# Kernel tuning notes

Hardware: AMD Instinct MI355X
Metric: run time of the kernel (lower is better)

## Reference

```python
import jax, jax.numpy as jnp
import numpy as np

K = 256  # k winners per row


def setup_inputs() -> dict:
    key = jax.random.key(0)
    k1, k2 = jax.random.split(key)
    x = jax.random.normal(k1, (32768, 2048), dtype=jnp.float32)
    importance = jax.random.normal(k2, (2048,), dtype=jnp.float32)
    return {"x": x, "importance": importance}


def reference(x, importance):
    # scores = |x| * |importance|  (broadcast over batch)
    scores = jnp.abs(x) * jnp.abs(importance)
    # top-k indices per row, then scatter 1.0 into a zero mask
    _, idx = jax.lax.top_k(scores, K)              # [B, K]
    rows = jnp.arange(x.shape[0])[:, None]          # [B, 1]
    mask = jnp.zeros_like(x).at[rows, idx].set(1.0)
    return x * mask
```

## Files before the change

### kernel.cpp

```cpp
#include <hip/hip_runtime.h>

#define COLS 2048
#define KSEL 256
#define TPB  256

#define WOFF  1024
#define BC    1028
#define BC2   1032
#define CNTW  1036
#define BUF   1040
#define R2O   1296
#define NWORDS 1360

__device__ __forceinline__ unsigned mbcnt64(unsigned long long m) {
    unsigned c = __builtin_amdgcn_mbcnt_lo((unsigned)m, 0u);
    return __builtin_amdgcn_mbcnt_hi((unsigned)(m >> 32), c);
}

__global__ __launch_bounds__(TPB)
void CompetitiveSelection_topk_kernel(const float* __restrict__ x,
                                      const float* __restrict__ imp,
                                      float* __restrict__ out)
{
    __shared__ __align__(16) unsigned lds[NWORDS];
    const int tid  = threadIdx.x;
    const int lane = tid & 63;
    const int wid  = tid >> 6;
    const long base = (long)blockIdx.x * COLS + tid * 8;

    *(uint4*)&lds[4 * tid] = make_uint4(0, 0, 0, 0);
    if (tid == 0) lds[CNTW] = 0;
    __syncthreads();

    float4 xa = *(const float4*)(x + base);
    float4 xb = *(const float4*)(x + base + 4);
    float4 ia = *(const float4*)(imp + tid * 8);
    float4 ib = *(const float4*)(imp + tid * 8 + 4);
    float xs[8] = {xa.x, xa.y, xa.z, xa.w, xb.x, xb.y, xb.z, xb.w};
    float iv[8] = {ia.x, ia.y, ia.z, ia.w, ib.x, ib.y, ib.z, ib.w};
    unsigned sc[8];
#pragma unroll
    for (int j = 0; j < 8; ++j) {
        sc[j] = __float_as_uint(xs[j] * iv[j]) & 0x7FFFFFFFu;
        atomicAdd(&lds[sc[j] >> 21], 1u);
    }
    __syncthreads();

    unsigned T = 0, kk = KSEL, na = 0;
    unsigned hm = 0x80000000u;
    int nb = 31;

    auto passScan = [&](int s) {
        uint4 h = *(const uint4*)&lds[4 * tid];
        unsigned cnt[4] = {h.x, h.y, h.z, h.w};
        unsigned tot = cnt[0] + cnt[1] + cnt[2] + cnt[3];
        unsigned S = tot;
#pragma unroll
        for (int off = 1; off < 64; off <<= 1) {
            unsigned u = __shfl_down(S, off);
            if (lane + off < 64) S += u;
        }
        if (lane == 0) lds[WOFF + wid] = S;
        __syncthreads();
        unsigned above = S - tot;
#pragma unroll
        for (int w = 0; w < 4; ++w) above += (w > wid) ? lds[WOFF + w] : 0u;
        int cc = -1; unsigned cab = 0, cnb = 0;
#pragma unroll
        for (int b = 3; b >= 0; --b) {
            if (cc < 0 && above < kk && above + cnt[b] >= kk) {
                cc = 4 * tid + b; cab = above; cnb = cnt[b];
            }
            above += cnt[b];
        }
        if (cc >= 0) {
            lds[BC + 0] = T | ((unsigned)cc << s);
            lds[BC + 1] = kk - cab;
            lds[BC + 2] = cnb;
        }
        __syncthreads();
        T = lds[BC + 0]; kk = lds[BC + 1]; na = lds[BC + 2];
        hm |= (0x3FFu << s);
        nb = s;
    };

    passScan(21);

    while (na > 256u && nb > 0) {
        int s = (nb > 10) ? (nb - 10) : 0;
        *(uint4*)&lds[4 * tid] = make_uint4(0, 0, 0, 0);
        __syncthreads();
#pragma unroll
        for (int j = 0; j < 8; ++j)
            if ((sc[j] & hm) == T) atomicAdd(&lds[(sc[j] >> s) & 1023u], 1u);
        __syncthreads();
        passScan(s);
    }

    unsigned ne, nlist = 0;
    if (nb == 0) {
        ne = na;
    } else {
        {
            unsigned c = 0;
#pragma unroll
            for (int j = 0; j < 8; ++j) c += ((sc[j] & hm) == T) ? 1u : 0u;
            unsigned S = c;
#pragma unroll
            for (int off = 1; off < 64; off <<= 1) {
                unsigned u = __shfl_up(S, off);
                if (lane >= off) S += u;
            }
            unsigned rb = 0;
            if (lane == 63) rb = atomicAdd(&lds[CNTW], S);
            unsigned p = BUF + __shfl(rb, 63) + S - c;
#pragma unroll
            for (int j = 0; j < 8; ++j)
                if ((sc[j] & hm) == T) lds[p++] = sc[j];
            nlist = na;
        }
        __syncthreads();

        while (na > 64u && nb > 0) {
            int s = (nb > 10) ? (nb - 10) : 0;
            *(uint4*)&lds[4 * tid] = make_uint4(0, 0, 0, 0);
            __syncthreads();
            for (int idx = tid; idx < (int)nlist; idx += TPB) {
                unsigned v = lds[BUF + idx];
                if ((v & hm) == T) atomicAdd(&lds[(v >> s) & 1023u], 1u);
            }
            __syncthreads();
            passScan(s);
        }

        if (nb == 0) {
            ne = na;
        } else {
            if (wid == 0) {
                unsigned run2 = 0;
                const unsigned nit = (nlist + 63u) >> 6;
                for (unsigned k = 0; k < nit; ++k) {
                    unsigned idx = (unsigned)lane + 64u * k;
                    bool inb = idx < nlist;
                    unsigned v = inb ? lds[BUF + idx] : 0u;
                    bool act = inb && ((v & hm) == T);
                    unsigned long long m = __ballot(act);
                    if (act) lds[R2O + run2 + mbcnt64(m)] = v;
                    run2 += (unsigned)__popcll(m);
                }
                unsigned v = ((unsigned)lane < na) ? lds[R2O + lane] : 0u;
                unsigned long long M = __ballot((unsigned)lane < na);
                unsigned tl = 0, k2 = kk;
                for (int b = nb - 1; b >= 0; --b) {
                    unsigned long long ones = __ballot((v >> b) & 1u) & M;
                    unsigned c1 = (unsigned)__popcll(ones);
                    if (c1 >= k2) { M = ones; tl |= (1u << b); }
                    else          { M &= ~ones; k2 -= c1; }
                }
                if (lane == 0) {
                    lds[BC2 + 0] = T | tl;
                    lds[BC2 + 1] = k2;
                    lds[BC2 + 2] = (unsigned)__popcll(M);
                }
            }
            __syncthreads();
            T = lds[BC2 + 0]; kk = lds[BC2 + 1]; ne = lds[BC2 + 2];
        }
    }

    float* orow = out + base;
    if (ne == kk) {
        float4 oa, ob;
        oa.x = (sc[0] >= T) ? xs[0] : 0.0f;
        oa.y = (sc[1] >= T) ? xs[1] : 0.0f;
        oa.z = (sc[2] >= T) ? xs[2] : 0.0f;
        oa.w = (sc[3] >= T) ? xs[3] : 0.0f;
        ob.x = (sc[4] >= T) ? xs[4] : 0.0f;
        ob.y = (sc[5] >= T) ? xs[5] : 0.0f;
        ob.z = (sc[6] >= T) ? xs[6] : 0.0f;
        ob.w = (sc[7] >= T) ? xs[7] : 0.0f;
        *(float4*)(orow)     = oa;
        *(float4*)(orow + 4) = ob;
    } else {
        unsigned eq = 0;
#pragma unroll
        for (int j = 0; j < 8; ++j) eq += (sc[j] == T) ? 1u : 0u;
        unsigned S = eq;
#pragma unroll
        for (int off = 1; off < 64; off <<= 1) {
            unsigned u = __shfl_up(S, off);
            if (lane >= off) S += u;
        }
        if (lane == 63) lds[WOFF + wid] = S;
        __syncthreads();
        unsigned add = 0;
#pragma unroll
        for (int w = 0; w < 4; ++w) add += (w < wid) ? lds[WOFF + w] : 0u;
        unsigned ebase = add + S - eq;
        float o[8];
#pragma unroll
        for (int j = 0; j < 8; ++j) {
            bool pick = sc[j] > T;
            if (sc[j] == T) { pick = (ebase < kk); ebase += 1; }
            o[j] = pick ? xs[j] : 0.0f;
        }
        *(float4*)(orow)     = make_float4(o[0], o[1], o[2], o[3]);
        *(float4*)(orow + 4) = make_float4(o[4], o[5], o[6], o[7]);
    }
}

extern "C" void kernel_launch(void* const* d_in, const int* in_sizes, int n_in,
                              void* d_out, int out_size, void* d_ws, size_t ws_size,
                              hipStream_t stream)
{
    const float* x   = (const float*)d_in[0];
    const float* imp = (const float*)d_in[1];
    float* out       = (float*)d_out;

    const int rows = in_sizes[0] / COLS;
    CompetitiveSelection_topk_kernel<<<dim3(rows), dim3(TPB), 0, stream>>>(x, imp, out);
}
```

Before: 111.4 us.

## Process two rows per block with interleaved radix-select passes

Each block now handles two rows, running their histogram and scan passes side by side so the two rows share barriers and have more independent work in flight. The refinement loop now stays on register-held scores until at most 64 candidates remain, dropping the intermediate LDS candidate list and the extra compaction step. The grid is halved. In exchange, registers per thread and LDS per block grow, and a row that needs more passes than its partner leaves that partner idle in the lockstep loop.

```diff
diff --git a/kernel.cpp b/kernel.cpp
--- a/kernel.cpp
+++ b/kernel.cpp
@@ -4,18 +4,19 @@
 #define KSEL 256
 #define TPB  256
 
-#define WOFF  1024
-#define BC    1028
-#define BC2   1032
-#define CNTW  1036
-#define BUF   1040
-#define R2O   1296
-#define NWORDS 1360
-
-__device__ __forceinline__ unsigned mbcnt64(unsigned long long m) {
-    unsigned c = __builtin_amdgcn_mbcnt_lo((unsigned)m, 0u);
-    return __builtin_amdgcn_mbcnt_hi((unsigned)(m >> 32), c);
-}
+#define HA    0
+#define HB    1024
+#define WOFFA 2048
+#define WOFFB 2052
+#define BCA   2056
+#define BCB   2060
+#define BC2A  2064
+#define BC2B  2068
+#define CA    2072
+#define CB    2073
+#define BUFA  2080
+#define BUFB  2144
+#define NWORDS 2208
 
 __global__ __launch_bounds__(TPB)
 void CompetitiveSelection_topk_kernel(const float* __restrict__ x,
@@ -26,186 +27,267 @@
     const int tid  = threadIdx.x;
     const int lane = tid & 63;
     const int wid  = tid >> 6;
-    const long base = (long)blockIdx.x * COLS + tid * 8;
-
-    *(uint4*)&lds[4 * tid] = make_uint4(0, 0, 0, 0);
-    if (tid == 0) lds[CNTW] = 0;
+    const long baseA = (long)(2 * blockIdx.x) * COLS + tid * 8;
+    const long baseB = baseA + COLS;
+
+    const uint4 z4 = make_uint4(0, 0, 0, 0);
+    *(uint4*)&lds[HA + 4 * tid] = z4;
+    *(uint4*)&lds[HB + 4 * tid] = z4;
+    if (tid < 2) lds[CA + tid] = 0;
     __syncthreads();
 
-    float4 xa = *(const float4*)(x + base);
-    float4 xb = *(const float4*)(x + base + 4);
-    float4 ia = *(const float4*)(imp + tid * 8);
-    float4 ib = *(const float4*)(imp + tid * 8 + 4);
-    float xs[8] = {xa.x, xa.y, xa.z, xa.w, xb.x, xb.y, xb.z, xb.w};
-    float iv[8] = {ia.x, ia.y, ia.z, ia.w, ib.x, ib.y, ib.z, ib.w};
-    unsigned sc[8];
+    float4 a0 = *(const float4*)(x + baseA);
+    float4 a1 = *(const float4*)(x + baseA + 4);
+    float4 b0 = *(const float4*)(x + baseB);
+    float4 b1 = *(const float4*)(x + baseB + 4);
+    float4 i0 = *(const float4*)(imp + tid * 8);
+    float4 i1 = *(const float4*)(imp + tid * 8 + 4);
+    float xsA[8] = {a0.x, a0.y, a0.z, a0.w, a1.x, a1.y, a1.z, a1.w};
+    float xsB[8] = {b0.x, b0.y, b0.z, b0.w, b1.x, b1.y, b1.z, b1.w};
+    float ivv[8] = {i0.x, i0.y, i0.z, i0.w, i1.x, i1.y, i1.z, i1.w};
+    unsigned scA[8], scB[8];
 #pragma unroll
     for (int j = 0; j < 8; ++j) {
-        sc[j] = __float_as_uint(xs[j] * iv[j]) & 0x7FFFFFFFu;
-        atomicAdd(&lds[sc[j] >> 21], 1u);
+        scA[j] = __float_as_uint(xsA[j] * ivv[j]) & 0x7FFFFFFFu;
+        scB[j] = __float_as_uint(xsB[j] * ivv[j]) & 0x7FFFFFFFu;
+        atomicAdd(&lds[HA + (scA[j] >> 21)], 1u);
+        atomicAdd(&lds[HB + (scB[j] >> 21)], 1u);
     }
     __syncthreads();
 
-    unsigned T = 0, kk = KSEL, na = 0;
-    unsigned hm = 0x80000000u;
-    int nb = 31;
-
-    auto passScan = [&](int s) {
-        uint4 h = *(const uint4*)&lds[4 * tid];
-        unsigned cnt[4] = {h.x, h.y, h.z, h.w};
-        unsigned tot = cnt[0] + cnt[1] + cnt[2] + cnt[3];
-        unsigned S = tot;
-#pragma unroll
-        for (int off = 1; off < 64; off <<= 1) {
-            unsigned u = __shfl_down(S, off);
-            if (lane + off < 64) S += u;
-        }
-        if (lane == 0) lds[WOFF + wid] = S;
-        __syncthreads();
-        unsigned above = S - tot;
-#pragma unroll
-        for (int w = 0; w < 4; ++w) above += (w > wid) ? lds[WOFF + w] : 0u;
-        int cc = -1; unsigned cab = 0, cnb = 0;
-#pragma unroll
-        for (int b = 3; b >= 0; --b) {
-            if (cc < 0 && above < kk && above + cnt[b] >= kk) {
-                cc = 4 * tid + b; cab = above; cnb = cnt[b];
-            }
-            above += cnt[b];
-        }
-        if (cc >= 0) {
-            lds[BC + 0] = T | ((unsigned)cc << s);
-            lds[BC + 1] = kk - cab;
-            lds[BC + 2] = cnb;
-        }
-        __syncthreads();
-        T = lds[BC + 0]; kk = lds[BC + 1]; na = lds[BC + 2];
-        hm |= (0x3FFu << s);
-        nb = s;
+    unsigned TA = 0, kkA = KSEL, naA = 0, hmA = 0x80000000u;
+    unsigned TB = 0, kkB = KSEL, naB = 0, hmB = 0x80000000u;
+    int nbA = 31, nbB = 31;
+
+    auto scanBoth = [&](bool actA, int sA, bool actB, int sB) {
+        uint4 hA4, hB4; unsigned SA = 0, SB = 0, totA = 0, totB = 0;
+        if (actA) {
+            hA4 = *(const uint4*)&lds[HA + 4 * tid];
+            totA = hA4.x + hA4.y + hA4.z + hA4.w; SA = totA;
+#pragma unroll
+            for (int off = 1; off < 64; off <<= 1) {
+                unsigned u = __shfl_down(SA, off);
+                if (lane + off < 64) SA += u;
+            }
+            if (lane == 0) lds[WOFFA + wid] = SA;
+        }
+        if (actB) {
+            hB4 = *(const uint4*)&lds[HB + 4 * tid];
+            totB = hB4.x + hB4.y + hB4.z + hB4.w; SB = totB;
+#pragma unroll
+            for (int off = 1; off < 64; off <<= 1) {
+                unsigned u = __shfl_down(SB, off);
+                if (lane + off < 64) SB += u;
+            }
+            if (lane == 0) lds[WOFFB + wid] = SB;
+        }
+        __syncthreads();
+        if (actA) {
+            unsigned above = SA - totA;
+#pragma unroll
+            for (int w = 0; w < 4; ++w) above += (w > wid) ? lds[WOFFA + w] : 0u;
+            unsigned cnt[4] = {hA4.x, hA4.y, hA4.z, hA4.w};
+            int cc = -1; unsigned cab = 0, cnb = 0;
+#pragma unroll
+            for (int b = 3; b >= 0; --b) {
+                if (cc < 0 && above < kkA && above + cnt[b] >= kkA) {
+                    cc = 4 * tid + b; cab = above; cnb = cnt[b];
+                }
+                above += cnt[b];
+            }
+            if (cc >= 0) {
+                lds[BCA + 0] = TA | ((unsigned)cc << sA);
+                lds[BCA + 1] = kkA - cab;
+                lds[BCA + 2] = cnb;
+            }
+        }
+        if (actB) {
+            unsigned above = SB - totB;
+#pragma unroll
+            for (int w = 0; w < 4; ++w) above += (w > wid) ? lds[WOFFB + w] : 0u;
+            unsigned cnt[4] = {hB4.x, hB4.y, hB4.z, hB4.w};
+            int cc = -1; unsigned cab = 0, cnb = 0;
+#pragma unroll
+            for (int b = 3; b >= 0; --b) {
+                if (cc < 0 && above < kkB && above + cnt[b] >= kkB) {
+                    cc = 4 * tid + b; cab = above; cnb = cnt[b];
+                }
+                above += cnt[b];
+            }
+            if (cc >= 0) {
+                lds[BCB + 0] = TB | ((unsigned)cc << sB);
+                lds[BCB + 1] = kkB - cab;
+                lds[BCB + 2] = cnb;
+            }
+        }
+        __syncthreads();
+        if (actA) { TA = lds[BCA]; kkA = lds[BCA + 1]; naA = lds[BCA + 2];
+                    hmA |= (0x3FFu << sA); nbA = sA; }
+        if (actB) { TB = lds[BCB]; kkB = lds[BCB + 1]; naB = lds[BCB + 2];
+                    hmB |= (0x3FFu << sB); nbB = sB; }
     };
 
-    passScan(21);
-
-    while (na > 256u && nb > 0) {
-        int s = (nb > 10) ? (nb - 10) : 0;
-        *(uint4*)&lds[4 * tid] = make_uint4(0, 0, 0, 0);
-        __syncthreads();
-#pragma unroll
-        for (int j = 0; j < 8; ++j)
-            if ((sc[j] & hm) == T) atomicAdd(&lds[(sc[j] >> s) & 1023u], 1u);
-        __syncthreads();
-        passScan(s);
-    }
-
-    unsigned ne, nlist = 0;
-    if (nb == 0) {
-        ne = na;
-    } else {
-        {
-            unsigned c = 0;
-#pragma unroll
-            for (int j = 0; j < 8; ++j) c += ((sc[j] & hm) == T) ? 1u : 0u;
-            unsigned S = c;
-#pragma unroll
-            for (int off = 1; off < 64; off <<= 1) {
-                unsigned u = __shfl_up(S, off);
-                if (lane >= off) S += u;
-            }
-            unsigned rb = 0;
-            if (lane == 63) rb = atomicAdd(&lds[CNTW], S);
-            unsigned p = BUF + __shfl(rb, 63) + S - c;
+    scanBoth(true, 21, true, 21);
+
+    while ((naA > 64u && nbA > 0) || (naB > 64u && nbB > 0)) {
+        bool rA = naA > 64u && nbA > 0, rB = naB > 64u && nbB > 0;
+        int sA2 = (nbA > 10) ? nbA - 10 : 0, sB2 = (nbB > 10) ? nbB - 10 : 0;
+        if (rA) *(uint4*)&lds[HA + 4 * tid] = z4;
+        if (rB) *(uint4*)&lds[HB + 4 * tid] = z4;
+        __syncthreads();
+        if (rA) {
 #pragma unroll
             for (int j = 0; j < 8; ++j)
-                if ((sc[j] & hm) == T) lds[p++] = sc[j];
-            nlist = na;
-        }
-        __syncthreads();
-
-        while (na > 64u && nb > 0) {
-            int s = (nb > 10) ? (nb - 10) : 0;
-            *(uint4*)&lds[4 * tid] = make_uint4(0, 0, 0, 0);
-            __syncthreads();
-            for (int idx = tid; idx < (int)nlist; idx += TPB) {
-                unsigned v = lds[BUF + idx];
-                if ((v & hm) == T) atomicAdd(&lds[(v >> s) & 1023u], 1u);
-            }
-            __syncthreads();
-            passScan(s);
-        }
-
-        if (nb == 0) {
-            ne = na;
-        } else {
-            if (wid == 0) {
-                unsigned run2 = 0;
-                const unsigned nit = (nlist + 63u) >> 6;
-                for (unsigned k = 0; k < nit; ++k) {
-                    unsigned idx = (unsigned)lane + 64u * k;
-                    bool inb = idx < nlist;
-                    unsigned v = inb ? lds[BUF + idx] : 0u;
-                    bool act = inb && ((v & hm) == T);
-                    unsigned long long m = __ballot(act);
-                    if (act) lds[R2O + run2 + mbcnt64(m)] = v;
-                    run2 += (unsigned)__popcll(m);
-                }
-                unsigned v = ((unsigned)lane < na) ? lds[R2O + lane] : 0u;
-                unsigned long long M = __ballot((unsigned)lane < na);
-                unsigned tl = 0, k2 = kk;
-                for (int b = nb - 1; b >= 0; --b) {
-                    unsigned long long ones = __ballot((v >> b) & 1u) & M;
-                    unsigned c1 = (unsigned)__popcll(ones);
-                    if (c1 >= k2) { M = ones; tl |= (1u << b); }
-                    else          { M &= ~ones; k2 -= c1; }
-                }
-                if (lane == 0) {
-                    lds[BC2 + 0] = T | tl;
-                    lds[BC2 + 1] = k2;
-                    lds[BC2 + 2] = (unsigned)__popcll(M);
-                }
-            }
-            __syncthreads();
-            T = lds[BC2 + 0]; kk = lds[BC2 + 1]; ne = lds[BC2 + 2];
-        }
-    }
-
-    float* orow = out + base;
-    if (ne == kk) {
-        float4 oa, ob;
-        oa.x = (sc[0] >= T) ? xs[0] : 0.0f;
-        oa.y = (sc[1] >= T) ? xs[1] : 0.0f;
-        oa.z = (sc[2] >= T) ? xs[2] : 0.0f;
-        oa.w = (sc[3] >= T) ? xs[3] : 0.0f;
-        ob.x = (sc[4] >= T) ? xs[4] : 0.0f;
-        ob.y = (sc[5] >= T) ? xs[5] : 0.0f;
-        ob.z = (sc[6] >= T) ? xs[6] : 0.0f;
-        ob.w = (sc[7] >= T) ? xs[7] : 0.0f;
-        *(float4*)(orow)     = oa;
-        *(float4*)(orow + 4) = ob;
-    } else {
-        unsigned eq = 0;
-#pragma unroll
-        for (int j = 0; j < 8; ++j) eq += (sc[j] == T) ? 1u : 0u;
-        unsigned S = eq;
+                if ((scA[j] & hmA) == TA)
+                    atomicAdd(&lds[HA + ((scA[j] >> sA2) & 1023u)], 1u);
+        }
+        if (rB) {
+#pragma unroll
+            for (int j = 0; j < 8; ++j)
+                if ((scB[j] & hmB) == TB)
+                    atomicAdd(&lds[HB + ((scB[j] >> sB2) & 1023u)], 1u);
+        }
+        __syncthreads();
+        scanBoth(rA, sA2, rB, sB2);
+    }
+
+    if (nbA > 0) {
+        unsigned c = 0;
+#pragma unroll
+        for (int j = 0; j < 8; ++j) c += ((scA[j] & hmA) == TA) ? 1u : 0u;
+        unsigned S = c;
 #pragma unroll
         for (int off = 1; off < 64; off <<= 1) {
             unsigned u = __shfl_up(S, off);
             if (lane >= off) S += u;
         }
-        if (lane == 63) lds[WOFF + wid] = S;
-        __syncthreads();
-        unsigned add = 0;
-#pragma unroll
-        for (int w = 0; w < 4; ++w) add += (w < wid) ? lds[WOFF + w] : 0u;
-        unsigned ebase = add + S - eq;
-        float o[8];
+        unsigned rb = 0;
+        if (lane == 63) rb = atomicAdd(&lds[CA], S);
+        unsigned p = BUFA + __shfl(rb, 63) + S - c;
+#pragma unroll
+        for (int j = 0; j < 8; ++j)
+            if ((scA[j] & hmA) == TA) lds[p++] = scA[j];
+    }
+    if (nbB > 0) {
+        unsigned c = 0;
+#pragma unroll
+        for (int j = 0; j < 8; ++j) c += ((scB[j] & hmB) == TB) ? 1u : 0u;
+        unsigned S = c;
+#pragma unroll
+        for (int off = 1; off < 64; off <<= 1) {
+            unsigned u = __shfl_up(S, off);
+            if (lane >= off) S += u;
+        }
+        unsigned rb = 0;
+        if (lane == 63) rb = atomicAdd(&lds[CB], S);
+        unsigned p = BUFB + __shfl(rb, 63) + S - c;
+#pragma unroll
+        for (int j = 0; j < 8; ++j)
+            if ((scB[j] & hmB) == TB) lds[p++] = scB[j];
+    }
+    __syncthreads();
+
+    if (wid == 0 && nbA > 0) {
+        unsigned v = ((unsigned)lane < naA) ? lds[BUFA + lane] : 0u;
+        unsigned long long M = __ballot((unsigned)lane < naA);
+        unsigned tl = 0, k2 = kkA;
+        for (int b = nbA - 1; b >= 0; --b) {
+            unsigned long long ones = __ballot((v >> b) & 1u) & M;
+            unsigned c1 = (unsigned)__popcll(ones);
+            if (c1 >= k2) { M = ones; tl |= (1u << b); }
+            else          { M &= ~ones; k2 -= c1; }
+        }
+        if (lane == 0) {
+            lds[BC2A + 0] = TA | tl;
+            lds[BC2A + 1] = k2;
+            lds[BC2A + 2] = (unsigned)__popcll(M);
+        }
+    }
+    if (wid == 1 && nbB > 0) {
+        unsigned v = ((unsigned)lane < naB) ? lds[BUFB + lane] : 0u;
+        unsigned long long M = __ballot((unsigned)lane < naB);
+        unsigned tl = 0, k2 = kkB;
+        for (int b = nbB - 1; b >= 0; --b) {
+            unsigned long long ones = __ballot((v >> b) & 1u) & M;
+            unsigned c1 = (unsigned)__popcll(ones);
+            if (c1 >= k2) { M = ones; tl |= (1u << b); }
+            else          { M &= ~ones; k2 -= c1; }
+        }
+        if (lane == 0) {
+            lds[BC2B + 0] = TB | tl;
+            lds[BC2B + 1] = k2;
+            lds[BC2B + 2] = (unsigned)__popcll(M);
+        }
+    }
+    __syncthreads();
+    unsigned neA, neB;
+    if (nbA > 0) { TA = lds[BC2A]; kkA = lds[BC2A + 1]; neA = lds[BC2A + 2]; }
+    else         { neA = naA; }
+    if (nbB > 0) { TB = lds[BC2B]; kkB = lds[BC2B + 1]; neB = lds[BC2B + 2]; }
+    else         { neB = naB; }
+
+    float* oA = out + baseA;
+    float* oB = out + baseB;
+    if (neA == kkA && neB == kkB) {
+        float4 p0, p1, q0, q1;
+        p0.x = (scA[0] >= TA) ? xsA[0] : 0.0f;
+        p0.y = (scA[1] >= TA) ? xsA[1] : 0.0f;
+        p0.z = (scA[2] >= TA) ? xsA[2] : 0.0f;
+        p0.w = (scA[3] >= TA) ? xsA[3] : 0.0f;
+        p1.x = (scA[4] >= TA) ? xsA[4] : 0.0f;
+        p1.y = (scA[5] >= TA) ? xsA[5] : 0.0f;
+        p1.z = (scA[6] >= TA) ? xsA[6] : 0.0f;
+        p1.w = (scA[7] >= TA) ? xsA[7] : 0.0f;
+        q0.x = (scB[0] >= TB) ? xsB[0] : 0.0f;
+        q0.y = (scB[1] >= TB) ? xsB[1] : 0.0f;
+        q0.z = (scB[2] >= TB) ? xsB[2] : 0.0f;
+        q0.w = (scB[3] >= TB) ? xsB[3] : 0.0f;
+        q1.x = (scB[4] >= TB) ? xsB[4] : 0.0f;
+        q1.y = (scB[5] >= TB) ? xsB[5] : 0.0f;
+        q1.z = (scB[6] >= TB) ? xsB[6] : 0.0f;
+        q1.w = (scB[7] >= TB) ? xsB[7] : 0.0f;
+        *(float4*)(oA)     = p0;
+        *(float4*)(oA + 4) = p1;
+        *(float4*)(oB)     = q0;
+        *(float4*)(oB + 4) = q1;
+    } else {
+        unsigned eqA = 0, eqB = 0;
 #pragma unroll
         for (int j = 0; j < 8; ++j) {
-            bool pick = sc[j] > T;
-            if (sc[j] == T) { pick = (ebase < kk); ebase += 1; }
-            o[j] = pick ? xs[j] : 0.0f;
-        }
-        *(float4*)(orow)     = make_float4(o[0], o[1], o[2], o[3]);
-        *(float4*)(orow + 4) = make_float4(o[4], o[5], o[6], o[7]);
+            eqA += (scA[j] == TA) ? 1u : 0u;
+            eqB += (scB[j] == TB) ? 1u : 0u;
+        }
+        unsigned SA = eqA, SB = eqB;
+#pragma unroll
+        for (int off = 1; off < 64; off <<= 1) {
+            unsigned uA = __shfl_up(SA, off);
+            unsigned uB = __shfl_up(SB, off);
+            if (lane >= off) { SA += uA; SB += uB; }
+        }
+        if (lane == 63) { lds[WOFFA + wid] = SA; lds[WOFFB + wid] = SB; }
+        __syncthreads();
+        unsigned addA = 0, addB = 0;
+#pragma unroll
+        for (int w = 0; w < 4; ++w) {
+            addA += (w < wid) ? lds[WOFFA + w] : 0u;
+            addB += (w < wid) ? lds[WOFFB + w] : 0u;
+        }
+        unsigned ebA = addA + SA - eqA;
+        unsigned ebB = addB + SB - eqB;
+        float o[8], p[8];
+#pragma unroll
+        for (int j = 0; j < 8; ++j) {
+            bool pickA = scA[j] > TA;
+            if (scA[j] == TA) { pickA = (ebA < kkA); ebA += 1; }
+            o[j] = pickA ? xsA[j] : 0.0f;
+            bool pickB = scB[j] > TB;
+            if (scB[j] == TB) { pickB = (ebB < kkB); ebB += 1; }
+            p[j] = pickB ? xsB[j] : 0.0f;
+        }
+        *(float4*)(oA)     = make_float4(o[0], o[1], o[2], o[3]);
+        *(float4*)(oA + 4) = make_float4(o[4], o[5], o[6], o[7]);
+        *(float4*)(oB)     = make_float4(p[0], p[1], p[2], p[3]);
+        *(float4*)(oB + 4) = make_float4(p[4], p[5], p[6], p[7]);
     }
 }
 
@@ -218,5 +300,5 @@
     float* out       = (float*)d_out;
 
     const int rows = in_sizes[0] / COLS;
-    CompetitiveSelection_topk_kernel<<<dim3(rows), dim3(TPB), 0, stream>>>(x, imp, out);
+    CompetitiveSelection_topk_kernel<<<dim3(rows / 2), dim3(TPB), 0, stream>>>(x, imp, out);
 }
```

Measured after the change: 134.1 us. +20.3%, slower.
